# Kernel tuning notes

Hardware: AMD Instinct MI355X
Metric: run time of the kernel (lower is better)

## Reference

```python
import jax, jax.numpy as jnp
import numpy as np

B, S, D = 4, 1024, 1024
E, F, TOPK = 16, 512, 4


def setup_inputs() -> dict:
    key = jax.random.key(0)
    k1, k2, k3, k4, k5 = jax.random.split(key, 5)
    scale = 0.02
    return {
        "x": jax.random.normal(k1, (B, S, D), dtype=jnp.float32),
        "Wr": jax.random.normal(k2, (D, E), dtype=jnp.float32) * scale,   # router
        "Wg": jax.random.normal(k3, (E, D, F), dtype=jnp.float32) * scale,  # gate proj
        "Wu": jax.random.normal(k4, (E, D, F), dtype=jnp.float32) * scale,  # up proj
        "Wd": jax.random.normal(k5, (E, F, D), dtype=jnp.float32) * scale,  # down proj
    }


def reference(x, Wr, Wg, Wu, Wd):
    b, s, d = x.shape
    xf = x.reshape(-1, d)                      # [N, D], N = B*S
    n = xf.shape[0]
    e = Wr.shape[1]

    # --- router: softmax over experts, top-k, renormalized weights ---
    probs = jax.nn.softmax(xf @ Wr, axis=-1)   # [N, E]
    w, idx = jax.lax.top_k(probs, TOPK)        # [N, K], [N, K]
    w = w / jnp.sum(w, axis=-1, keepdims=True)

    # combine weights per (token, expert); zero for unselected experts.
    # Equivalent to the per-expert where/gather/scatter-add loop in torch.
    cw = jnp.zeros((n, e), dtype=xf.dtype).at[jnp.arange(n)[:, None], idx].add(w)

    # --- per-expert gated FFN (SwiGLU), combined with routing weights ---
    def body(acc, ws):
        wg, wu, wd, c = ws                     # [D,F], [D,F], [F,D], [N]
        h = jax.nn.silu(xf @ wg) * (xf @ wu)   # [N, F]
        return acc + c[:, None] * (h @ wd), None

    out, _ = jax.lax.scan(body, jnp.zeros_like(xf), (Wg, Wu, Wd, cw.T))
    return out.reshape(b, s, d)
```

## Files before the change

### kernel.cpp

```cpp
#include <hip/hip_runtime.h>

#define N_TOK 4096
#define DIM   1024
#define NE    16
#define NF    512
#define TOPK  4
#define CAP   4096
#define NPAIR (N_TOK * TOPK)
#define MAXTILES 144
#define GU_BLOCKS (8 * MAXTILES)
#define DN_BLOCKS (8 * MAXTILES)
#define PREPD_BLOCKS (NE * 128)
#define RP_ROUTER 1024
#define RP_PREP   4096

typedef _Float16 v8h __attribute__((ext_vector_type(8)));
typedef float    v4f __attribute__((ext_vector_type(4)));

__device__ __forceinline__ void prep_tile(
    const float* __restrict__ src, unsigned short* __restrict__ dst,
    int R, int C, int RIL, int e, int cbl, int rbl, float (*tile)[65])
{
    int c0 = cbl * 64, r0 = rbl * 64;
    const float* s = src + (size_t)e * R * C;
    int t = threadIdx.x;
    int tr = t >> 4, tc = (t & 15) * 4;
#pragma unroll
    for (int i = 0; i < 4; i++) {
        int row = i * 16 + tr;
        float4 v = *(const float4*)(s + (size_t)(r0 + row) * C + c0 + tc);
        tile[row][tc + 0] = v.x; tile[row][tc + 1] = v.y;
        tile[row][tc + 2] = v.z; tile[row][tc + 3] = v.w;
    }
    __syncthreads();
    int ktPerE = R >> 5;
    int cbPerE = C >> RIL;
    int imgSz  = (1 << RIL) * 32;
#pragma unroll
    for (int i = 0; i < 4; i++) {
        int nr = i * 16 + tr;
        int orow = c0 + nr;
        int k0 = r0 + tc;
        int cb = orow >> RIL;
        int r  = orow & ((1 << RIL) - 1);
        int kt = k0 >> 5;
        size_t off = ((size_t)(e * cbPerE + cb) * ktPerE + kt) * imgSz
                   + r * 32 + (k0 & 31);
        union { unsigned short u[4]; uint2 v; } p;
#pragma unroll
        for (int j = 0; j < 4; j++)
            p.u[j] = __builtin_bit_cast(unsigned short, (_Float16)tile[tc + j][nr]);
        *(uint2*)(dst + off) = p.v;
    }
}

__global__ __launch_bounds__(256) void router_prep_kernel(
    const float* __restrict__ x, const float* __restrict__ Wr,
    const float* __restrict__ Wg, const float* __restrict__ Wu,
    int* __restrict__ tokIdx, float* __restrict__ tokW,
    unsigned short* __restrict__ xb,
    unsigned short* __restrict__ Wg_t, unsigned short* __restrict__ Wu_t)
{
    __shared__ __align__(16) float tile[64][65];
    int bid = blockIdx.x;
    if (bid >= RP_ROUTER) {
        int pid = bid - RP_ROUTER;
        int z = pid >> 7;
        int which = z >> 4, e = z & 15;
        int bx = pid & 127;
        int cbl = bx & 7, rbl = bx >> 3;
        prep_tile(which ? Wu : Wg, which ? Wu_t : Wg_t,
                  DIM, NF, 6, e, cbl, rbl, tile);
        return;
    }
    int tid = threadIdx.x;
    int w = tid >> 6, l = tid & 63;
    int t = bid * 4 + w;

    double z[NE];
#pragma unroll
    for (int e = 0; e < NE; e++) z[e] = 0.0;
    const float* xrow = x + (size_t)t * DIM;
#pragma unroll
    for (int i = 0; i < 16; i++) {
        int d = i * 64 + l;
        double xv = (double)xrow[d];
        const float4* wr = (const float4*)(Wr + d * NE);
        float4 w0 = wr[0], w1 = wr[1], w2 = wr[2], w3 = wr[3];
        z[0]  += xv * w0.x; z[1]  += xv * w0.y; z[2]  += xv * w0.z; z[3]  += xv * w0.w;
        z[4]  += xv * w1.x; z[5]  += xv * w1.y; z[6]  += xv * w1.z; z[7]  += xv * w1.w;
        z[8]  += xv * w2.x; z[9]  += xv * w2.y; z[10] += xv * w2.z; z[11] += xv * w2.w;
        z[12] += xv * w3.x; z[13] += xv * w3.y; z[14] += xv * w3.z; z[15] += xv * w3.w;
    }
    const float4* xv4 = (const float4*)xrow;
#pragma unroll
    for (int h2 = 0; h2 < 2; h2++) {
        int base = h2 * 512 + l * 8;
        float4 a = xv4[h2 * 128 + l * 2];
        float4 b = xv4[h2 * 128 + l * 2 + 1];
        union { unsigned short u[8]; uint4 v; } p;
        p.u[0] = __builtin_bit_cast(unsigned short, (_Float16)a.x);
        p.u[1] = __builtin_bit_cast(unsigned short, (_Float16)a.y);
        p.u[2] = __builtin_bit_cast(unsigned short, (_Float16)a.z);
        p.u[3] = __builtin_bit_cast(unsigned short, (_Float16)a.w);
        p.u[4] = __builtin_bit_cast(unsigned short, (_Float16)b.x);
        p.u[5] = __builtin_bit_cast(unsigned short, (_Float16)b.y);
        p.u[6] = __builtin_bit_cast(unsigned short, (_Float16)b.z);
        p.u[7] = __builtin_bit_cast(unsigned short, (_Float16)b.w);
        *(uint4*)(xb + (size_t)t * DIM + base) = p.v;
    }
#pragma unroll
    for (int e = 0; e < NE; e++) {
#pragma unroll
        for (int m = 1; m < 64; m <<= 1) z[e] += __shfl_xor(z[e], m, 64);
    }
    if (l == 0) {
        bool taken[NE];
#pragma unroll
        for (int e = 0; e < NE; e++) taken[e] = false;
        int idx[TOPK]; double sel[TOPK];
        for (int k = 0; k < TOPK; k++) {
            int bi = 0; double bv = -1.0e300;
            for (int e = 0; e < NE; e++)
                if (!taken[e] && z[e] > bv) { bv = z[e]; bi = e; }
            taken[bi] = true; idx[k] = bi; sel[k] = bv;
        }
        double m = sel[0];
        double ex[TOPK]; double s = 0.0;
        for (int k = 0; k < TOPK; k++) { ex[k] = exp(sel[k] - m); s += ex[k]; }
        for (int k = 0; k < TOPK; k++) {
            tokIdx[t * TOPK + k] = idx[k];
            tokW[t * TOPK + k]   = (float)(ex[k] / s);
        }
    }
}

__global__ __launch_bounds__(256) void bin_kernel(
    const int* __restrict__ tokIdx,
    int* __restrict__ cnt, int* __restrict__ bpair)
{
    int e = blockIdx.x;
    int tid = threadIdx.x, lane = tid & 63, wv = tid >> 6;
    __shared__ int wsum[4];
    __shared__ int sbase;
    if (tid == 0) sbase = 0;
    __syncthreads();
    unsigned long long lt = (1ULL << lane) - 1ULL;
#pragma unroll 1
    for (int c0 = 0; c0 < NPAIR; c0 += 1024) {
        int i0 = c0 + tid * 4;
        int4 v = *(const int4*)(tokIdx + i0);
        int m[4] = {v.x == e, v.y == e, v.z == e, v.w == e};
        int r[4]; int wcnt = 0;
#pragma unroll
        for (int j = 0; j < 4; j++) {
            unsigned long long bal = __ballot(m[j] != 0);
            r[j] = wcnt + __popcll(bal & lt);
            wcnt += __popcll(bal);
        }
        if (lane == 0) wsum[wv] = wcnt;
        __syncthreads();
        int woff = sbase;
        for (int k = 0; k < wv; k++) woff += wsum[k];
#pragma unroll
        for (int j = 0; j < 4; j++)
            if (m[j]) bpair[e * CAP + woff + r[j]] = i0 + j;
        __syncthreads();
        if (tid == 0) sbase += wsum[0] + wsum[1] + wsum[2] + wsum[3];
        __syncthreads();
    }
    if (tid == 0) cnt[e] = sbase;
}

__device__ __forceinline__ int ldsw(int row, int chunk) {
    return row * 32 + (chunk ^ ((row >> 1) & 3)) * 8;
}

__device__ __forceinline__ void gload16(const unsigned short* g, unsigned short* l) {
    __builtin_amdgcn_global_load_lds(
        (const __attribute__((address_space(1))) void*)g,
        (__attribute__((address_space(3))) void*)l, 16, 0, 0);
}

__device__ __forceinline__ bool find_tile(const int* __restrict__ cnt,
                                          int ti, int& e, int& mt, int& tbase) {
    int rt = 0;
#pragma unroll 1
    for (int ee = 0; ee < NE; ee++) {
        int nt = (cnt[ee] + 127) >> 7;
        if (ti < rt + nt) { e = ee; mt = ti - rt; tbase = rt; return true; }
        rt += nt;
    }
    return false;
}

__global__ __launch_bounds__(256) void ffn_gate_up_kernel(
    const unsigned short* __restrict__ xb,
    const unsigned short* __restrict__ Wg_t,
    const unsigned short* __restrict__ Wu_t,
    const int* __restrict__ cnt,
    const int* __restrict__ bpair,
    unsigned short* __restrict__ h_t,
    const float* __restrict__ Wd,
    unsigned short* __restrict__ Wd_t)
{
    __shared__ __align__(16) unsigned char smem[49152];
    unsigned short* sX = (unsigned short*)smem;
    unsigned short* sG = (unsigned short*)(smem + 24576);
    unsigned short* sU = (unsigned short*)(smem + 36864);
    float (*tile)[65] = (float (*)[65])smem;

    int bid = blockIdx.x;
    if (bid >= GU_BLOCKS) {
        int pid = bid - GU_BLOCKS;
        int e = pid >> 7;
        int bx = pid & 127;
        int cbl = bx & 15, rbl = bx >> 4;
        prep_tile(Wd, Wd_t, NF, DIM, 7, e, cbl, rbl, tile);
        return;
    }
    int xcd = bid & 7, q = bid >> 3;
    int ti = xcd * 18 + (q >> 3);
    int fb = q & 7;
    int e, mt, tbase;
    if (!find_tile(cnt, ti, e, mt, tbase)) return;
    int count = cnt[e];

    int tid = threadIdx.x, lane = tid & 63, w = tid >> 6;

    int srow0 = w * 16 + (lane >> 2);
    int srow1 = srow0 + 64;
    int spos  = lane & 3;
    int cx0 = spos ^ ((srow0 >> 1) & 3);
    int cx1 = spos ^ ((srow1 >> 1) & 3);
    int tok0 = bpair[e * CAP + min(mt * 128 + srow0, count - 1)] >> 2;
    int tok1 = bpair[e * CAP + min(mt * 128 + srow1, count - 1)] >> 2;
    const unsigned short* gX0 = xb + (size_t)tok0 * DIM + cx0 * 8;
    const unsigned short* gX1 = xb + (size_t)tok1 * DIM + cx1 * 8;
    const unsigned short* gG  = Wg_t + ((size_t)(e * 8 + fb) * 32) * 2048 + srow0 * 32 + cx0 * 8;
    const unsigned short* gU  = Wu_t + ((size_t)(e * 8 + fb) * 32) * 2048 + srow0 * 32 + cx0 * 8;
    unsigned short* dX0 = sX + (size_t)(w * 16) * 32;
    unsigned short* dX1 = sX + (size_t)(64 + w * 16) * 32;
    unsigned short* dG  = sG + (size_t)(w * 16) * 32;
    unsigned short* dU  = sU + (size_t)(w * 16) * 32;

    int row = lane & 15, q2 = lane >> 4;
    int rw = w & 1, cw = w >> 1;
    int aoff[4], goff[2];
#pragma unroll
    for (int mi = 0; mi < 4; mi++) aoff[mi] = ldsw(rw * 64 + mi * 16 + row, q2);
#pragma unroll
    for (int ni = 0; ni < 2; ni++) goff[ni] = ldsw(cw * 32 + ni * 16 + row, q2);

    v4f accG[4][2], accU[4][2];
    v4f zero = {0.f, 0.f, 0.f, 0.f};
#pragma unroll
    for (int mi = 0; mi < 4; mi++)
#pragma unroll
        for (int ni = 0; ni < 2; ni++) { accG[mi][ni] = zero; accU[mi][ni] = zero; }

#define STAGE_GU(b, kt) do {                                   \
        gload16(gX0 + (kt) * 32, dX0 + (b) * 4096);            \
        gload16(gX1 + (kt) * 32, dX1 + (b) * 4096);            \
        gload16(gG + (size_t)(kt) * 2048, dG + (b) * 2048);    \
        gload16(gU + (size_t)(kt) * 2048, dU + (b) * 2048);    \
    } while (0)

    STAGE_GU(0, 0);
    STAGE_GU(1, 1);

#pragma unroll 1
    for (int kt = 0; kt < 32; kt++) {
        int buf = kt % 3;
        if (kt < 30) {
            STAGE_GU((kt + 2) % 3, kt + 2);
            asm volatile("s_waitcnt vmcnt(8)" ::: "memory");
        } else if (kt == 30) {
            asm volatile("s_waitcnt vmcnt(4)" ::: "memory");
        } else {
            asm volatile("s_waitcnt vmcnt(0)" ::: "memory");
        }
        __builtin_amdgcn_s_barrier();
        __builtin_amdgcn_sched_barrier(0);
        const unsigned short* bX = sX + buf * 4096;
        const unsigned short* bGp = sG + buf * 2048;
        const unsigned short* bUp = sU + buf * 2048;
        v8h a[4], bg[2], bu[2];
#pragma unroll
        for (int mi = 0; mi < 4; mi++) a[mi] = *(const v8h*)&bX[aoff[mi]];
#pragma unroll
        for (int ni = 0; ni < 2; ni++) {
            bg[ni] = *(const v8h*)&bGp[goff[ni]];
            bu[ni] = *(const v8h*)&bUp[goff[ni]];
        }
#pragma unroll
        for (int mi = 0; mi < 4; mi++)
#pragma unroll
            for (int ni = 0; ni < 2; ni++) {
                accG[mi][ni] = __builtin_amdgcn_mfma_f32_16x16x32_f16(a[mi], bg[ni], accG[mi][ni], 0, 0, 0);
                accU[mi][ni] = __builtin_amdgcn_mfma_f32_16x16x32_f16(a[mi], bu[ni], accU[mi][ni], 0, 0, 0);
            }
        __builtin_amdgcn_sched_barrier(0);
        __builtin_amdgcn_s_barrier();
        __builtin_amdgcn_sched_barrier(0);
    }
#undef STAGE_GU

    size_t himg = (size_t)(tbase + mt) * 16;
#pragma unroll
    for (int mi = 0; mi < 4; mi++)
#pragma unroll
        for (int ni = 0; ni < 2; ni++) {
            int f = fb * 64 + cw * 32 + ni * 16 + row;
#pragma unroll
            for (int i = 0; i < 4; i++) {
                int rl = rw * 64 + mi * 16 + q2 * 4 + i;
                int pos = mt * 128 + rl;
                if (pos < count) {
                    float gv = accG[mi][ni][i];
                    float uv = accU[mi][ni][i];
                    float hv = gv * uv / (1.0f + __expf(-gv));
                    size_t off = (himg + (f >> 5)) * 4096 + rl * 32 + (f & 31);
                    h_t[off] = __builtin_bit_cast(unsigned short, (_Float16)hv);
                }
            }
        }
}

__global__ __launch_bounds__(256) void ffn_down_kernel(
    const unsigned short* __restrict__ h_t,
    const unsigned short* __restrict__ Wd_t,
    const int* __restrict__ cnt,
    const int* __restrict__ bpair,
    unsigned short* __restrict__ part)
{
    int bid = blockIdx.x;
    int xcd = bid & 7, q = bid >> 3;
    int ti = xcd * 18 + (q >> 3);
    int db = q & 7;
    int e, mt, tbase;
    if (!find_tile(cnt, ti, e, mt, tbase)) return;
    int count = cnt[e];

    __shared__ __align__(16) unsigned short sH[3 * 128 * 32];
    __shared__ __align__(16) unsigned short sW[3 * 128 * 32];

    int tid = threadIdx.x, lane = tid & 63, w = tid >> 6;

    int srow0 = w * 16 + (lane >> 2);
    int srow1 = srow0 + 64;
    int spos  = lane & 3;
    int c0 = spos ^ ((srow0 >> 1) & 3);
    int c1 = spos ^ ((srow1 >> 1) & 3);
    const unsigned short* hbase = h_t + ((size_t)(tbase + mt) * 16) * 4096;
    const unsigned short* wbase = Wd_t + ((size_t)(e * 8 + db) * 16) * 4096;
    const unsigned short* gH0 = hbase + srow0 * 32 + c0 * 8;
    const unsigned short* gH1 = hbase + srow1 * 32 + c1 * 8;
    const unsigned short* gW0 = wbase + srow0 * 32 + c0 * 8;
    const unsigned short* gW1 = wbase + srow1 * 32 + c1 * 8;
    unsigned short* dH0 = sH + (size_t)(w * 16) * 32;
    unsigned short* dH1 = sH + (size_t)(64 + w * 16) * 32;
    unsigned short* dW0 = sW + (size_t)(w * 16) * 32;
    unsigned short* dW1 = sW + (size_t)(64 + w * 16) * 32;

    int row = lane & 15, q2 = lane >> 4;
    int rw = w & 1, cw = w >> 1;
    int aoff[4], boff[4];
#pragma unroll
    for (int mi = 0; mi < 4; mi++) aoff[mi] = ldsw(rw * 64 + mi * 16 + row, q2);
#pragma unroll
    for (int ni = 0; ni < 4; ni++) boff[ni] = ldsw(cw * 64 + ni * 16 + row, q2);

    v4f acc[4][4];
    v4f zero = {0.f, 0.f, 0.f, 0.f};
#pragma unroll
    for (int mi = 0; mi < 4; mi++)
#pragma unroll
        for (int ni = 0; ni < 4; ni++) acc[mi][ni] = zero;

#define STAGE_D(b, kt) do {                                         \
        gload16(gH0 + (size_t)(kt) * 4096, dH0 + (b) * 4096);       \
        gload16(gH1 + (size_t)(kt) * 4096, dH1 + (b) * 4096);       \
        gload16(gW0 + (size_t)(kt) * 4096, dW0 + (b) * 4096);       \
        gload16(gW1 + (size_t)(kt) * 4096, dW1 + (b) * 4096);       \
    } while (0)

    STAGE_D(0, 0);
    STAGE_D(1, 1);

#pragma unroll 1
    for (int kt = 0; kt < 16; kt++) {
        int buf = kt % 3;
        if (kt < 14) {
            STAGE_D((kt + 2) % 3, kt + 2);
            asm volatile("s_waitcnt vmcnt(8)" ::: "memory");
        } else if (kt == 14) {
            asm volatile("s_waitcnt vmcnt(4)" ::: "memory");
        } else {
            asm volatile("s_waitcnt vmcnt(0)" ::: "memory");
        }
        __builtin_amdgcn_s_barrier();
        __builtin_amdgcn_sched_barrier(0);
        const unsigned short* bH = sH + buf * 4096;
        const unsigned short* bW = sW + buf * 4096;
        v8h a[4], b[4];
#pragma unroll
        for (int mi = 0; mi < 4; mi++) a[mi] = *(const v8h*)&bH[aoff[mi]];
#pragma unroll
        for (int ni = 0; ni < 4; ni++) b[ni] = *(const v8h*)&bW[boff[ni]];
#pragma unroll
        for (int mi = 0; mi < 4; mi++)
#pragma unroll
            for (int ni = 0; ni < 4; ni++)
                acc[mi][ni] = __builtin_amdgcn_mfma_f32_16x16x32_f16(a[mi], b[ni], acc[mi][ni], 0, 0, 0);
        __builtin_amdgcn_sched_barrier(0);
        __builtin_amdgcn_s_barrier();
        __builtin_amdgcn_sched_barrier(0);
    }
#undef STAGE_D

#pragma unroll
    for (int mi = 0; mi < 4; mi++)
#pragma unroll
        for (int i = 0; i < 4; i++) {
            int rl = rw * 64 + mi * 16 + q2 * 4 + i;
            int pos = mt * 128 + rl;
            if (pos < count) {
                int p = bpair[e * CAP + pos];
#pragma unroll
                for (int ni = 0; ni < 4; ni++) {
                    int col = db * 128 + cw * 64 + ni * 16 + row;
                    part[(size_t)p * DIM + col] =
                        __builtin_bit_cast(unsigned short, (_Float16)acc[mi][ni][i]);
                }
            }
        }
}

__global__ __launch_bounds__(256) void combine_kernel(
    const unsigned short* __restrict__ part, const float* __restrict__ tokW,
    float* __restrict__ out)
{
    int gid = blockIdx.x * 256 + threadIdx.x;
    int t = gid >> 8;
    int c = (gid & 255) * 4;
    float4 r = {0.f, 0.f, 0.f, 0.f};
#pragma unroll
    for (int k = 0; k < TOPK; k++) {
        float wk = tokW[t * TOPK + k];
        union { uint2 u; _Float16 h[4]; } cv;
        cv.u = *(const uint2*)(part + ((size_t)(t * TOPK + k)) * DIM + c);
        r.x += wk * (float)cv.h[0];
        r.y += wk * (float)cv.h[1];
        r.z += wk * (float)cv.h[2];
        r.w += wk * (float)cv.h[3];
    }
    *(float4*)(out + (size_t)t * DIM + c) = r;
}

extern "C" void kernel_launch(void* const* d_in, const int* in_sizes, int n_in,
                              void* d_out, int out_size, void* d_ws, size_t ws_size,
                              hipStream_t stream)
{
    const float* x  = (const float*)d_in[0];
    const float* Wr = (const float*)d_in[1];
    const float* Wg = (const float*)d_in[2];
    const float* Wu = (const float*)d_in[3];
    const float* Wd = (const float*)d_in[4];
    float* out = (float*)d_out;
    char* ws = (char*)d_ws;

    size_t off = 0;
    int* tokIdx = (int*)(ws + off);   off += (size_t)NPAIR * 4;
    float* tokW = (float*)(ws + off); off += (size_t)NPAIR * 4;
    int* cnt    = (int*)(ws + off);   off += 256;
    int* bpair  = (int*)(ws + off);   off += (size_t)NE * CAP * 4;
    unsigned short* xb   = (unsigned short*)(ws + off); off += (size_t)N_TOK * DIM * 2;
    unsigned short* Wg_t = (unsigned short*)(ws + off); off += (size_t)NE * DIM * NF * 2;
    unsigned short* Wu_t = (unsigned short*)(ws + off); off += (size_t)NE * DIM * NF * 2;
    unsigned short* Wd_t = (unsigned short*)(ws + off); off += (size_t)NE * DIM * NF * 2;
    unsigned short* h_t  = (unsigned short*)(ws + off); off += (size_t)MAXTILES * 16 * 4096 * 2;
    unsigned short* part = (unsigned short*)(ws + off); off += (size_t)NPAIR * DIM * 2;

    router_prep_kernel<<<RP_ROUTER + RP_PREP, 256, 0, stream>>>(
        x, Wr, Wg, Wu, tokIdx, tokW, xb, Wg_t, Wu_t);
    bin_kernel<<<NE, 256, 0, stream>>>(tokIdx, cnt, bpair);
    ffn_gate_up_kernel<<<GU_BLOCKS + PREPD_BLOCKS, 256, 0, stream>>>(
        xb, Wg_t, Wu_t, cnt, bpair, h_t, Wd, Wd_t);
    ffn_down_kernel<<<DN_BLOCKS, 256, 0, stream>>>(
        h_t, Wd_t, cnt, bpair, part);
    combine_kernel<<<(N_TOK * DIM) / (256 * 4), 256, 0, stream>>>(part, tokW, out);
}
```

Before: 269.9 us.

## Switch down-proj to double-buffered LDS pipeline and widen combine loads

The down-projection kernel goes from a 3-stage LDS ring with explicit vmcnt waits to a 2-stage double buffer. Each iteration issues the next tile's async loads and then ends with a __syncthreads. This lowers LDS use, which may allow more resident blocks, but leaves less prefetch distance to hide global-load latency. The combine kernel now has each thread handle 8 halves with 16-byte loads instead of 4, halving the thread count. There is a risk that relying on __syncthreads to cover outstanding global-to-LDS loads gives weaker ordering than the explicit waitcnt did.

```diff
diff --git a/kernel.cpp b/kernel.cpp
--- a/kernel.cpp
+++ b/kernel.cpp
@@ -342,8 +342,8 @@
     if (!find_tile(cnt, ti, e, mt, tbase)) return;
     int count = cnt[e];
 
-    __shared__ __align__(16) unsigned short sH[3 * 128 * 32];
-    __shared__ __align__(16) unsigned short sW[3 * 128 * 32];
+    __shared__ __align__(16) unsigned short sH[2 * 128 * 32];
+    __shared__ __align__(16) unsigned short sW[2 * 128 * 32];
 
     int tid = threadIdx.x, lane = tid & 63, w = tid >> 6;
 
@@ -386,21 +386,12 @@
     } while (0)
 
     STAGE_D(0, 0);
-    STAGE_D(1, 1);
+    __syncthreads();
 
 #pragma unroll 1
     for (int kt = 0; kt < 16; kt++) {
-        int buf = kt % 3;
-        if (kt < 14) {
-            STAGE_D((kt + 2) % 3, kt + 2);
-            asm volatile("s_waitcnt vmcnt(8)" ::: "memory");
-        } else if (kt == 14) {
-            asm volatile("s_waitcnt vmcnt(4)" ::: "memory");
-        } else {
-            asm volatile("s_waitcnt vmcnt(0)" ::: "memory");
-        }
-        __builtin_amdgcn_s_barrier();
-        __builtin_amdgcn_sched_barrier(0);
+        int buf = kt & 1;
+        if (kt < 15) STAGE_D(buf ^ 1, kt + 1);
         const unsigned short* bH = sH + buf * 4096;
         const unsigned short* bW = sW + buf * 4096;
         v8h a[4], b[4];
@@ -413,9 +404,7 @@
 #pragma unroll
             for (int ni = 0; ni < 4; ni++)
                 acc[mi][ni] = __builtin_amdgcn_mfma_f32_16x16x32_f16(a[mi], b[ni], acc[mi][ni], 0, 0, 0);
-        __builtin_amdgcn_sched_barrier(0);
-        __builtin_amdgcn_s_barrier();
-        __builtin_amdgcn_sched_barrier(0);
+        __syncthreads();
     }
 #undef STAGE_D
 
@@ -442,20 +431,19 @@
     float* __restrict__ out)
 {
     int gid = blockIdx.x * 256 + threadIdx.x;
-    int t = gid >> 8;
-    int c = (gid & 255) * 4;
-    float4 r = {0.f, 0.f, 0.f, 0.f};
+    int t = gid >> 7;
+    int c = (gid & 127) * 8;
+    float r[8] = {0.f, 0.f, 0.f, 0.f, 0.f, 0.f, 0.f, 0.f};
 #pragma unroll
     for (int k = 0; k < TOPK; k++) {
         float wk = tokW[t * TOPK + k];
-        union { uint2 u; _Float16 h[4]; } cv;
-        cv.u = *(const uint2*)(part + ((size_t)(t * TOPK + k)) * DIM + c);
-        r.x += wk * (float)cv.h[0];
-        r.y += wk * (float)cv.h[1];
-        r.z += wk * (float)cv.h[2];
-        r.w += wk * (float)cv.h[3];
-    }
-    *(float4*)(out + (size_t)t * DIM + c) = r;
+        union { uint4 u; _Float16 h[8]; } cv;
+        cv.u = *(const uint4*)(part + ((size_t)(t * TOPK + k)) * DIM + c);
+#pragma unroll
+        for (int j = 0; j < 8; j++) r[j] += wk * (float)cv.h[j];
+    }
+    *(float4*)(out + (size_t)t * DIM + c)     = *(float4*)&r[0];
+    *(float4*)(out + (size_t)t * DIM + c + 4) = *(float4*)&r[4];
 }
 
 extern "C" void kernel_launch(void* const* d_in, const int* in_sizes, int n_in,
@@ -489,5 +477,5 @@
         xb, Wg_t, Wu_t, cnt, bpair, h_t, Wd, Wd_t);
     ffn_down_kernel<<<DN_BLOCKS, 256, 0, stream>>>(
         h_t, Wd_t, cnt, bpair, part);
-    combine_kernel<<<(N_TOK * DIM) / (256 * 4), 256, 0, stream>>>(part, tokW, out);
-}
+    combine_kernel<<<(N_TOK * DIM) / (256 * 8), 256, 0, stream>>>(part, tokW, out);
+}
```

Result: no change. 269.5 us (-0.1%).
